# Optimization experiments

Hardware: AMD Instinct MI355X
Metric: run time of the kernel (lower is better)

## Reference

```python
import jax, jax.numpy as jnp
import numpy as np

TEMPERATURE = 8.0

def setup_inputs() -> dict:
    key = jax.random.key(0)
    kq, kk, kv, km = jax.random.split(key, 4)
    B, H, S, D = 4, 16, 2048, 64
    q = jax.random.normal(kq, (B, H, S, D), dtype=jnp.float32)
    k = jax.random.normal(kk, (B, H, S, D), dtype=jnp.float32)
    v = jax.random.normal(kv, (B, H, S, D), dtype=jnp.float32)
    mask = jax.random.randint(km, (B, S, S), 0, 2, dtype=jnp.int32)
    return {"q": q, "k": k, "v": v, "mask": mask}

def reference(q, k, v, mask):
    # attn = q @ k^T / temperature  -> [B, H, Sq, Sk]
    attn = jnp.einsum("bhqd,bhkd->bhqk", q, k) / TEMPERATURE
    mask0 = (mask == 0)[:, None, :, :]  # [B, 1, Sq, Sk]; True where masked out
    attn = jnp.where(mask0, -jnp.inf, attn)
    attn = jax.nn.softmax(attn, axis=-1)
    attn = jnp.where(mask0, 0.0, attn)
    output = jnp.einsum("bhqk,bhkd->bhqd", attn, v)
    return (output, attn)
```

## Files before the change

kernel.cpp:

```cpp
#include <hip/hip_runtime.h>
#include <cstdint>

#define B_ 4
#define H_ 16
#define S_ 2048
#define D_ 64

#define QSCALE (0.125f * 1.44269504088896f)

typedef _Float16 half8 __attribute__((ext_vector_type(8)));
typedef float f32x4 __attribute__((ext_vector_type(4)));
typedef float f32x16 __attribute__((ext_vector_type(16)));
typedef uint32_t u32x2 __attribute__((ext_vector_type(2)));
typedef uint32_t u32x4 __attribute__((ext_vector_type(4)));


__global__ void cvt_q_kernel(const float* __restrict__ q, _Float16* __restrict__ qh) {
    const int64_t N = (int64_t)B_ * H_ * S_ * D_;
    const int64_t step = (int64_t)gridDim.x * blockDim.x * 4;
    for (int64_t i = ((int64_t)blockIdx.x * blockDim.x + threadIdx.x) * 4; i < N; i += step) {
        float4 a = *reinterpret_cast<const float4*>(q + i);
        _Float16 ah[4] = { (_Float16)(a.x * QSCALE), (_Float16)(a.y * QSCALE),
                           (_Float16)(a.z * QSCALE), (_Float16)(a.w * QSCALE) };
        *reinterpret_cast<u32x2*>(qh + i) = *reinterpret_cast<u32x2*>(ah);
    }
}

__global__ void pack_k_kernel(const float* __restrict__ k, _Float16* __restrict__ kh) {
    const int bh = blockIdx.y;
    const int t = blockIdx.x;
    const int tid = threadIdx.x;
    const int kk = tid >> 6, lane = tid & 63, hi = lane >> 5, c = lane & 31;
    const float* src = k + ((int64_t)bh * S_ + t * 32 + c) * D_ + kk * 16 + hi * 8;
    float4 a = *reinterpret_cast<const float4*>(src);
    float4 b2 = *reinterpret_cast<const float4*>(src + 4);
    half8 h = { (_Float16)a.x, (_Float16)a.y, (_Float16)a.z, (_Float16)a.w,
                (_Float16)b2.x, (_Float16)b2.y, (_Float16)b2.z, (_Float16)b2.w };
    half8* dst = reinterpret_cast<half8*>(kh) + (((int64_t)bh * 64 + t) * 4 + kk) * 64 + hi * 32 + c;
    *dst = h;
}

__global__ void pack_v_kernel(const float* __restrict__ v, _Float16* __restrict__ vt) {
    const int bh = blockIdx.y;
    const int t = blockIdx.x;
    const int tid = threadIdx.x;
    const int g = tid >> 5, c = tid & 31;
    const int kk = g >> 2, hi = (g >> 1) & 1, db = g & 1;
    const float* src = v + ((int64_t)bh * S_ + t * 32 + kk * 16 + hi * 8) * D_ + c + 32 * db;
    half8 h;
#pragma unroll
    for (int j = 0; j < 8; ++j) h[j] = (_Float16)src[j * D_];
    half8* dst = reinterpret_cast<half8*>(vt) + (((int64_t)bh * 64 + t) * 8 + g) * 32 + c;
    *dst = h;
}

__global__ void pack_mask_kernel(const int* __restrict__ mask, uint32_t* __restrict__ mbits) {
    const int64_t groups = (int64_t)B_ * S_ * S_ / 64;
    const int lane = threadIdx.x & 63;
    const int64_t wstep = ((int64_t)gridDim.x * blockDim.x) >> 6;
    for (int64_t g = ((int64_t)blockIdx.x * blockDim.x + threadIdx.x) >> 6; g < groups; g += wstep) {
        int mv = mask[g * 64 + lane];
        unsigned long long bits = __ballot(mv != 0);
        if (lane == 0)
            *reinterpret_cast<unsigned long long*>(mbits + g * 2) = bits;
    }
}


__global__ __launch_bounds__(256, 2) void attn_fast(
    const _Float16* __restrict__ qh, const _Float16* __restrict__ kh, const _Float16* __restrict__ vt,
    const uint32_t* __restrict__ mbits,
    float* __restrict__ out, float* __restrict__ attn)
{
    const int tid = threadIdx.x;
    const int w = tid >> 6;
    const int lane = tid & 63;
    const int c = lane & 31;
    const int hi = lane >> 5;

    const int fid = blockIdx.x;
    const int xcd = fid & 7;
    const int slot = fid >> 3;
    const int p = xcd + 8 * (slot >> 4);
    const int x = slot & 15;
    const int b = p >> 4;

    const int qw = x * 128 + w * 32;
    const int64_t bh = p;
    const int64_t qrow = (int64_t)b * S_ + qw + c;

    half8 aq[4];
    {
        const _Float16* qp = qh + (bh * S_ + qw + c) * D_ + hi * 8;
#pragma unroll
        for (int kk = 0; kk < 4; ++kk)
            aq[kk] = *reinterpret_cast<const half8*>(qp + kk * 16);
    }

    const uint32_t* mrow = mbits + qrow * (S_ / 32);
    const half8* kbase = reinterpret_cast<const half8*>(kh) + (int64_t)bh * 64 * 4 * 64 + hi * 32 + c;
    const half8* vbase = reinterpret_cast<const half8*>(vt) + (int64_t)bh * 64 * 8 * 32 + c;

    auto LOADK = [&](half8 (&kr)[4], int t) {
        const half8* kp8 = kbase + (int64_t)t * 256;
#pragma unroll
        for (int kk = 0; kk < 4; ++kk) kr[kk] = kp8[kk * 64];
    };
    auto LOADV = [&](half8 (&vr)[4], int t) {
        const half8* vp8 = vbase + (int64_t)t * 256;
        vr[0] = vp8[(hi * 2 + 0) * 32];
        vr[1] = vp8[(hi * 2 + 1) * 32];
        vr[2] = vp8[(4 + hi * 2 + 0) * 32];
        vr[3] = vp8[(4 + hi * 2 + 1) * 32];
    };
    auto QK = [&](const half8 (&kr)[4]) -> f32x16 {
        f32x16 acc;
#pragma unroll
        for (int r = 0; r < 16; ++r) acc[r] = 0.f;
#pragma unroll
        for (int kk = 0; kk < 4; ++kk)
            acc = __builtin_amdgcn_mfma_f32_32x32x16_f16(kr[kk], aq[kk], acc, 0, 0, 0);
        return acc;
    };

    float l = 0.f;
    {
        auto bodyA = [&](const half8 (&kr)[4], uint32_t mwf) -> float {
            f32x16 acc = QK(kr);
            const uint32_t mw = mwf >> (hi * 4);
            float e[16];
#pragma unroll
            for (int r = 0; r < 16; ++r) {
                const bool dead = ((mw >> ((r & 3) + 8 * (r >> 2))) & 1u) == 0u;
                e[r] = __builtin_exp2f(dead ? -1e30f : acc[r]);
            }
#pragma unroll
            for (int st = 1; st < 16; st <<= 1)
#pragma unroll
                for (int i = 0; i < 16; i += 2 * st) e[i] += e[i + st];
            return e[0];
        };

        half8 ka[4], kb[4];
        uint32_t mA, mB;
        LOADK(ka, 0); mA = mrow[0];
        for (int t = 0; t < 64; t += 2) {
            LOADK(kb, t + 1); mB = mrow[t + 1];
            l += bodyA(ka, mA);
            if (t + 2 < 64) { LOADK(ka, t + 2); mA = mrow[t + 2]; }
            l += bodyA(kb, mB);
        }
    }
    const float lt = l + __shfl_xor(l, 32);
    const float rinv = 1.0f / lt;

    f32x16 o0, o1;
#pragma unroll
    for (int r = 0; r < 16; ++r) { o0[r] = 0.f; o1[r] = 0.f; }

    {
        auto bodyB = [&](const half8 (&kr)[4], const half8 (&vr)[4], uint32_t mwf, int t) {
            const int k0 = t * 32;
            f32x16 acc = QK(kr);
            const uint32_t mw = mwf >> (hi * 4);

            f32x4 pq0, pq1, pq2, pq3;
            uint32_t pk[8];
            {
#pragma unroll
                for (int e2 = 0; e2 < 4; ++e2) {
                    bool d0 = ((mw >> (0 + e2)) & 1u) == 0u;
                    bool d1 = ((mw >> (8 + e2)) & 1u) == 0u;
                    bool d2 = ((mw >> (16 + e2)) & 1u) == 0u;
                    bool d3 = ((mw >> (24 + e2)) & 1u) == 0u;
                    pq0[e2] = __builtin_exp2f(d0 ? -1e30f : acc[e2]) * rinv;
                    pq1[e2] = __builtin_exp2f(d1 ? -1e30f : acc[4 + e2]) * rinv;
                    pq2[e2] = __builtin_exp2f(d2 ? -1e30f : acc[8 + e2]) * rinv;
                    pq3[e2] = __builtin_exp2f(d3 ? -1e30f : acc[12 + e2]) * rinv;
                }
                pk[0] = __builtin_bit_cast(uint32_t, __builtin_amdgcn_cvt_pkrtz(pq0[0], pq0[1]));
                pk[1] = __builtin_bit_cast(uint32_t, __builtin_amdgcn_cvt_pkrtz(pq0[2], pq0[3]));
                pk[2] = __builtin_bit_cast(uint32_t, __builtin_amdgcn_cvt_pkrtz(pq1[0], pq1[1]));
                pk[3] = __builtin_bit_cast(uint32_t, __builtin_amdgcn_cvt_pkrtz(pq1[2], pq1[3]));
                pk[4] = __builtin_bit_cast(uint32_t, __builtin_amdgcn_cvt_pkrtz(pq2[0], pq2[1]));
                pk[5] = __builtin_bit_cast(uint32_t, __builtin_amdgcn_cvt_pkrtz(pq2[2], pq2[3]));
                pk[6] = __builtin_bit_cast(uint32_t, __builtin_amdgcn_cvt_pkrtz(pq3[0], pq3[1]));
                pk[7] = __builtin_bit_cast(uint32_t, __builtin_amdgcn_cvt_pkrtz(pq3[2], pq3[3]));
            }

            u32x2 rA = __builtin_amdgcn_permlane32_swap(pk[0], pk[2], false, false);
            u32x2 rB = __builtin_amdgcn_permlane32_swap(pk[1], pk[3], false, false);
            u32x2 rC = __builtin_amdgcn_permlane32_swap(pk[4], pk[6], false, false);
            u32x2 rD = __builtin_amdgcn_permlane32_swap(pk[5], pk[7], false, false);
            u32x4 fa0 = { rA[0], rB[0], rA[1], rB[1] };
            u32x4 fa1 = { rC[0], rD[0], rC[1], rD[1] };
            half8 pa0 = __builtin_bit_cast(half8, fa0);
            half8 pa1 = __builtin_bit_cast(half8, fa1);

            o0 = __builtin_amdgcn_mfma_f32_32x32x16_f16(pa0, vr[0], o0, 0, 0, 0);
            o1 = __builtin_amdgcn_mfma_f32_32x32x16_f16(pa0, vr[1], o1, 0, 0, 0);
            o0 = __builtin_amdgcn_mfma_f32_32x32x16_f16(pa1, vr[2], o0, 0, 0, 0);
            o1 = __builtin_amdgcn_mfma_f32_32x32x16_f16(pa1, vr[3], o1, 0, 0, 0);

            float* arow = attn + (bh * S_ + qw + c) * (int64_t)S_ + k0 + 4 * hi;
            *reinterpret_cast<f32x4*>(arow) = pq0;
            *reinterpret_cast<f32x4*>(arow + 8) = pq1;
            *reinterpret_cast<f32x4*>(arow + 16) = pq2;
            *reinterpret_cast<f32x4*>(arow + 24) = pq3;
        };

        half8 ka[4], kb[4], va[4], vb[4];
        uint32_t mA, mB;
        LOADK(ka, 0); LOADV(va, 0); mA = mrow[0];
        for (int t = 0; t < 64; t += 2) {
            LOADK(kb, t + 1); LOADV(vb, t + 1); mB = mrow[t + 1];
            bodyB(ka, va, mA, t);
            if (t + 2 < 64) { LOADK(ka, t + 2); LOADV(va, t + 2); mA = mrow[t + 2]; }
            bodyB(kb, vb, mB, t + 1);
        }
    }

#pragma unroll
    for (int r = 0; r < 16; ++r) {
        const int row = (r & 3) + 8 * (r >> 2) + 4 * hi;
        float* op = out + (bh * S_ + qw + row) * D_;
        op[c] = o0[r];
        op[c + 32] = o1[r];
    }
}

__global__ __launch_bounds__(256, 2) void attn_slow(
    const float* __restrict__ qf, const float* __restrict__ kf, const float* __restrict__ vf,
    const int* __restrict__ maskI, float* __restrict__ out, float* __restrict__ attn)
{
    const int tid = threadIdx.x;
    const int w = tid >> 6;
    const int lane = tid & 63;
    const int c = lane & 31;
    const int hi = lane >> 5;
    const int fid = blockIdx.x;
    const int p = fid & 63;
    const int x = fid >> 6;
    const int b = p >> 4;
    const int qw = x * 128 + w * 32;
    const int64_t bh = p;
    const int64_t qrow = (int64_t)b * S_ + qw + c;

    half8 aq[4];
    {
        const float* qp = qf + (bh * S_ + qw + c) * D_ + hi * 8;
#pragma unroll
        for (int kk = 0; kk < 4; ++kk)
#pragma unroll
            for (int j = 0; j < 8; ++j)
                aq[kk][j] = (_Float16)(qp[kk * 16 + j] * QSCALE);
    }

    float l = 0.f;
    for (int t = 0; t < 64; ++t) {
        const int k0 = t * 32;
        f32x16 acc;
#pragma unroll
        for (int r = 0; r < 16; ++r) acc[r] = 0.f;
        const float* kp = kf + (bh * S_ + k0 + c) * D_ + hi * 8;
#pragma unroll
        for (int kk = 0; kk < 4; ++kk) {
            half8 bk;
#pragma unroll
            for (int j = 0; j < 8; ++j) bk[j] = (_Float16)kp[kk * 16 + j];
            acc = __builtin_amdgcn_mfma_f32_32x32x16_f16(bk, aq[kk], acc, 0, 0, 0);
        }
        float e[16];
#pragma unroll
        for (int r = 0; r < 16; ++r) {
            const int key = k0 + (r & 3) + 8 * (r >> 2) + 4 * hi;
            const bool dead = maskI[qrow * S_ + key] == 0;
            e[r] = __builtin_exp2f(dead ? -1e30f : acc[r]);
        }
#pragma unroll
        for (int st = 1; st < 16; st <<= 1)
#pragma unroll
            for (int i = 0; i < 16; i += 2 * st) e[i] += e[i + st];
        l += e[0];
    }
    const float lt = l + __shfl_xor(l, 32);
    const float rinv = 1.0f / lt;

    f32x16 o0, o1;
#pragma unroll
    for (int r = 0; r < 16; ++r) { o0[r] = 0.f; o1[r] = 0.f; }

    for (int t = 0; t < 64; ++t) {
        const int k0 = t * 32;
        f32x16 acc;
#pragma unroll
        for (int r = 0; r < 16; ++r) acc[r] = 0.f;
        const float* kp = kf + (bh * S_ + k0 + c) * D_ + hi * 8;
#pragma unroll
        for (int kk = 0; kk < 4; ++kk) {
            half8 bk;
#pragma unroll
            for (int j = 0; j < 8; ++j) bk[j] = (_Float16)kp[kk * 16 + j];
            acc = __builtin_amdgcn_mfma_f32_32x32x16_f16(bk, aq[kk], acc, 0, 0, 0);
        }
        float* arow = attn + (bh * S_ + qw + c) * (int64_t)S_ + k0 + 4 * hi;
        uint32_t pk[8];
#pragma unroll
        for (int g4 = 0; g4 < 4; ++g4) {
            f32x4 pq;
#pragma unroll
            for (int e2 = 0; e2 < 4; ++e2) {
                const int key = k0 + e2 + 8 * g4 + 4 * hi;
                const bool dead = maskI[qrow * S_ + key] == 0;
                pq[e2] = __builtin_exp2f(dead ? -1e30f : acc[4 * g4 + e2]) * rinv;
            }
            *reinterpret_cast<f32x4*>(arow + 8 * g4) = pq;
            pk[2 * g4]     = __builtin_bit_cast(uint32_t, __builtin_amdgcn_cvt_pkrtz(pq[0], pq[1]));
            pk[2 * g4 + 1] = __builtin_bit_cast(uint32_t, __builtin_amdgcn_cvt_pkrtz(pq[2], pq[3]));
        }
        u32x2 rA = __builtin_amdgcn_permlane32_swap(pk[0], pk[2], false, false);
        u32x2 rB = __builtin_amdgcn_permlane32_swap(pk[1], pk[3], false, false);
        u32x2 rC = __builtin_amdgcn_permlane32_swap(pk[4], pk[6], false, false);
        u32x2 rD = __builtin_amdgcn_permlane32_swap(pk[5], pk[7], false, false);
        u32x4 fa0 = { rA[0], rB[0], rA[1], rB[1] };
        u32x4 fa1 = { rC[0], rD[0], rC[1], rD[1] };
        half8 pa0 = __builtin_bit_cast(half8, fa0);
        half8 pa1 = __builtin_bit_cast(half8, fa1);

        half8 bv00, bv01, bv10, bv11;
        const float* vp0 = vf + (bh * S_ + k0 + hi * 8) * D_ + c;
        const float* vp1 = vp0 + 16 * D_;
#pragma unroll
        for (int j = 0; j < 8; ++j) {
            bv00[j] = (_Float16)vp0[j * D_];
            bv01[j] = (_Float16)vp0[j * D_ + 32];
            bv10[j] = (_Float16)vp1[j * D_];
            bv11[j] = (_Float16)vp1[j * D_ + 32];
        }
        o0 = __builtin_amdgcn_mfma_f32_32x32x16_f16(pa0, bv00, o0, 0, 0, 0);
        o1 = __builtin_amdgcn_mfma_f32_32x32x16_f16(pa0, bv01, o1, 0, 0, 0);
        o0 = __builtin_amdgcn_mfma_f32_32x32x16_f16(pa1, bv10, o0, 0, 0, 0);
        o1 = __builtin_amdgcn_mfma_f32_32x32x16_f16(pa1, bv11, o1, 0, 0, 0);
    }

#pragma unroll
    for (int r = 0; r < 16; ++r) {
        const int row = (r & 3) + 8 * (r >> 2) + 4 * hi;
        float* op = out + (bh * S_ + qw + row) * D_;
        op[c] = o0[r];
        op[c + 32] = o1[r];
    }
}

extern "C" void kernel_launch(void* const* d_in, const int* in_sizes, int n_in,
                              void* d_out, int out_size, void* d_ws, size_t ws_size,
                              hipStream_t stream) {
    const float* q = (const float*)d_in[0];
    const float* k = (const float*)d_in[1];
    const float* v = (const float*)d_in[2];
    const int* mask = (const int*)d_in[3];
    float* out = (float*)d_out;
    float* attn = out + (int64_t)B_ * H_ * S_ * D_;

    const size_t nElem = (size_t)B_ * H_ * S_ * D_;
    const size_t maskWords = (size_t)B_ * S_ * (S_ / 32);
    const size_t need = nElem * 2 * 3 + maskWords * 4;

    const int nblk = B_ * H_ * (S_ / 128);
    if (d_ws != nullptr && ws_size >= need) {
        _Float16* qh = (_Float16*)d_ws;
        _Float16* kh = qh + nElem;
        _Float16* vt = kh + nElem;
        uint32_t* mb = (uint32_t*)(vt + nElem);
        cvt_q_kernel<<<1024, 256, 0, stream>>>(q, qh);
        pack_k_kernel<<<dim3(S_ / 32, B_ * H_), 256, 0, stream>>>(k, kh);
        pack_v_kernel<<<dim3(S_ / 32, B_ * H_), 256, 0, stream>>>(v, vt);
        pack_mask_kernel<<<2048, 256, 0, stream>>>(mask, mb);
        attn_fast<<<nblk, 256, 0, stream>>>(qh, kh, vt, mb, out, attn);
    } else {
        attn_slow<<<nblk, 256, 0, stream>>>(q, k, v, mask, out, attn);
    }
}
```

Baseline: 546.1 us.

## Transpose packed mask bits for coalesced loads and deepen K/V prefetch pipeline

The packed mask is stored transposed so that, for each key tile, the 32 query-row words sit next to each other and a wavefront's mask loads coalesce instead of striding by the full row length. The first pass now keeps four K tiles and the second pass three K/V tiles in flight, issuing each next load right after the MFMAs rather than one tile ahead. The aim is to hide global-load latency behind compute in this bandwidth-heavy kernel. The cost is higher register pressure under launch_bounds(256,2), which could cause spills, plus a more scattered write pattern in the mask pack kernel.

Measured after the change: 545.4 us. Within noise of the previous version (-0.1%).

```diff
diff --git a/kernel.cpp b/kernel.cpp
--- a/kernel.cpp
+++ b/kernel.cpp
@@ -54,22 +54,29 @@
     *dst = h;
 }
 
-__global__ void pack_mask_kernel(const int* __restrict__ mask, uint32_t* __restrict__ mbits) {
+__global__ void pack_mask_kernel(const int* __restrict__ mask, uint32_t* __restrict__ mbT) {
     const int64_t groups = (int64_t)B_ * S_ * S_ / 64;
     const int lane = threadIdx.x & 63;
     const int64_t wstep = ((int64_t)gridDim.x * blockDim.x) >> 6;
     for (int64_t g = ((int64_t)blockIdx.x * blockDim.x + threadIdx.x) >> 6; g < groups; g += wstep) {
         int mv = mask[g * 64 + lane];
         unsigned long long bits = __ballot(mv != 0);
-        if (lane == 0)
-            *reinterpret_cast<unsigned long long*>(mbits + g * 2) = bits;
+        if (lane == 0) {
+            const int u = (int)(g & 31);
+            const int64_t bq = g >> 5;
+            const int q = (int)(bq & (S_ - 1));
+            const int b = (int)(bq >> 11);
+            const int64_t base = (((int64_t)b * 64 + (q >> 5)) * 64) * 32 + (q & 31);
+            mbT[base + (int64_t)(2 * u) * 32]     = (uint32_t)bits;
+            mbT[base + (int64_t)(2 * u + 1) * 32] = (uint32_t)(bits >> 32);
+        }
     }
 }
 
 
 __global__ __launch_bounds__(256, 2) void attn_fast(
     const _Float16* __restrict__ qh, const _Float16* __restrict__ kh, const _Float16* __restrict__ vt,
-    const uint32_t* __restrict__ mbits,
+    const uint32_t* __restrict__ mbT,
     float* __restrict__ out, float* __restrict__ attn)
 {
     const int tid = threadIdx.x;
@@ -87,7 +94,6 @@
 
     const int qw = x * 128 + w * 32;
     const int64_t bh = p;
-    const int64_t qrow = (int64_t)b * S_ + qw + c;
 
     half8 aq[4];
     {
@@ -97,7 +103,7 @@
             aq[kk] = *reinterpret_cast<const half8*>(qp + kk * 16);
     }
 
-    const uint32_t* mrow = mbits + qrow * (S_ / 32);
+    const uint32_t* mT = mbT + (((int64_t)b * 64 + x * 4 + w) * 64) * 32 + c;
     const half8* kbase = reinterpret_cast<const half8*>(kh) + (int64_t)bh * 64 * 4 * 64 + hi * 32 + c;
     const half8* vbase = reinterpret_cast<const half8*>(vt) + (int64_t)bh * 64 * 8 * 32 + c;
 
@@ -141,14 +147,17 @@
             return e[0];
         };
 
-        half8 ka[4], kb[4];
-        uint32_t mA, mB;
-        LOADK(ka, 0); mA = mrow[0];
-        for (int t = 0; t < 64; t += 2) {
-            LOADK(kb, t + 1); mB = mrow[t + 1];
-            l += bodyA(ka, mA);
-            if (t + 2 < 64) { LOADK(ka, t + 2); mA = mrow[t + 2]; }
-            l += bodyA(kb, mB);
+        half8 k0_[4], k1_[4], k2_[4], k3_[4];
+        uint32_t m0, m1, m2, m3;
+        LOADK(k0_, 0); m0 = mT[0 * 32];
+        LOADK(k1_, 1); m1 = mT[1 * 32];
+        LOADK(k2_, 2); m2 = mT[2 * 32];
+        LOADK(k3_, 3); m3 = mT[3 * 32];
+        for (int t = 0; t < 64; t += 4) {
+            l += bodyA(k0_, m0); if (t + 4 < 64) { LOADK(k0_, t + 4); m0 = mT[(t + 4) * 32]; }
+            l += bodyA(k1_, m1); if (t + 5 < 64) { LOADK(k1_, t + 5); m1 = mT[(t + 5) * 32]; }
+            l += bodyA(k2_, m2); if (t + 6 < 64) { LOADK(k2_, t + 6); m2 = mT[(t + 6) * 32]; }
+            l += bodyA(k3_, m3); if (t + 7 < 64) { LOADK(k3_, t + 7); m3 = mT[(t + 7) * 32]; }
         }
     }
     const float lt = l + __shfl_xor(l, 32);
@@ -159,34 +168,32 @@
     for (int r = 0; r < 16; ++r) { o0[r] = 0.f; o1[r] = 0.f; }
 
     {
-        auto bodyB = [&](const half8 (&kr)[4], const half8 (&vr)[4], uint32_t mwf, int t) {
+        auto stepB = [&](half8 (&K)[4], half8 (&V)[4], uint32_t& m_, int t, int tn) {
             const int k0 = t * 32;
-            f32x16 acc = QK(kr);
-            const uint32_t mw = mwf >> (hi * 4);
+            f32x16 acc = QK(K);
+            const uint32_t mw = m_ >> (hi * 4);
 
             f32x4 pq0, pq1, pq2, pq3;
             uint32_t pk[8];
-            {
-#pragma unroll
-                for (int e2 = 0; e2 < 4; ++e2) {
-                    bool d0 = ((mw >> (0 + e2)) & 1u) == 0u;
-                    bool d1 = ((mw >> (8 + e2)) & 1u) == 0u;
-                    bool d2 = ((mw >> (16 + e2)) & 1u) == 0u;
-                    bool d3 = ((mw >> (24 + e2)) & 1u) == 0u;
-                    pq0[e2] = __builtin_exp2f(d0 ? -1e30f : acc[e2]) * rinv;
-                    pq1[e2] = __builtin_exp2f(d1 ? -1e30f : acc[4 + e2]) * rinv;
-                    pq2[e2] = __builtin_exp2f(d2 ? -1e30f : acc[8 + e2]) * rinv;
-                    pq3[e2] = __builtin_exp2f(d3 ? -1e30f : acc[12 + e2]) * rinv;
-                }
-                pk[0] = __builtin_bit_cast(uint32_t, __builtin_amdgcn_cvt_pkrtz(pq0[0], pq0[1]));
-                pk[1] = __builtin_bit_cast(uint32_t, __builtin_amdgcn_cvt_pkrtz(pq0[2], pq0[3]));
-                pk[2] = __builtin_bit_cast(uint32_t, __builtin_amdgcn_cvt_pkrtz(pq1[0], pq1[1]));
-                pk[3] = __builtin_bit_cast(uint32_t, __builtin_amdgcn_cvt_pkrtz(pq1[2], pq1[3]));
-                pk[4] = __builtin_bit_cast(uint32_t, __builtin_amdgcn_cvt_pkrtz(pq2[0], pq2[1]));
-                pk[5] = __builtin_bit_cast(uint32_t, __builtin_amdgcn_cvt_pkrtz(pq2[2], pq2[3]));
-                pk[6] = __builtin_bit_cast(uint32_t, __builtin_amdgcn_cvt_pkrtz(pq3[0], pq3[1]));
-                pk[7] = __builtin_bit_cast(uint32_t, __builtin_amdgcn_cvt_pkrtz(pq3[2], pq3[3]));
+#pragma unroll
+            for (int e2 = 0; e2 < 4; ++e2) {
+                bool d0 = ((mw >> (0 + e2)) & 1u) == 0u;
+                bool d1 = ((mw >> (8 + e2)) & 1u) == 0u;
+                bool d2 = ((mw >> (16 + e2)) & 1u) == 0u;
+                bool d3 = ((mw >> (24 + e2)) & 1u) == 0u;
+                pq0[e2] = __builtin_exp2f(d0 ? -1e30f : acc[e2]) * rinv;
+                pq1[e2] = __builtin_exp2f(d1 ? -1e30f : acc[4 + e2]) * rinv;
+                pq2[e2] = __builtin_exp2f(d2 ? -1e30f : acc[8 + e2]) * rinv;
+                pq3[e2] = __builtin_exp2f(d3 ? -1e30f : acc[12 + e2]) * rinv;
             }
+            pk[0] = __builtin_bit_cast(uint32_t, __builtin_amdgcn_cvt_pkrtz(pq0[0], pq0[1]));
+            pk[1] = __builtin_bit_cast(uint32_t, __builtin_amdgcn_cvt_pkrtz(pq0[2], pq0[3]));
+            pk[2] = __builtin_bit_cast(uint32_t, __builtin_amdgcn_cvt_pkrtz(pq1[0], pq1[1]));
+            pk[3] = __builtin_bit_cast(uint32_t, __builtin_amdgcn_cvt_pkrtz(pq1[2], pq1[3]));
+            pk[4] = __builtin_bit_cast(uint32_t, __builtin_amdgcn_cvt_pkrtz(pq2[0], pq2[1]));
+            pk[5] = __builtin_bit_cast(uint32_t, __builtin_amdgcn_cvt_pkrtz(pq2[2], pq2[3]));
+            pk[6] = __builtin_bit_cast(uint32_t, __builtin_amdgcn_cvt_pkrtz(pq3[0], pq3[1]));
+            pk[7] = __builtin_bit_cast(uint32_t, __builtin_amdgcn_cvt_pkrtz(pq3[2], pq3[3]));
 
             u32x2 rA = __builtin_amdgcn_permlane32_swap(pk[0], pk[2], false, false);
             u32x2 rB = __builtin_amdgcn_permlane32_swap(pk[1], pk[3], false, false);
@@ -197,10 +204,12 @@
             half8 pa0 = __builtin_bit_cast(half8, fa0);
             half8 pa1 = __builtin_bit_cast(half8, fa1);
 
-            o0 = __builtin_amdgcn_mfma_f32_32x32x16_f16(pa0, vr[0], o0, 0, 0, 0);
-            o1 = __builtin_amdgcn_mfma_f32_32x32x16_f16(pa0, vr[1], o1, 0, 0, 0);
-            o0 = __builtin_amdgcn_mfma_f32_32x32x16_f16(pa1, vr[2], o0, 0, 0, 0);
-            o1 = __builtin_amdgcn_mfma_f32_32x32x16_f16(pa1, vr[3], o1, 0, 0, 0);
+            o0 = __builtin_amdgcn_mfma_f32_32x32x16_f16(pa0, V[0], o0, 0, 0, 0);
+            o1 = __builtin_amdgcn_mfma_f32_32x32x16_f16(pa0, V[1], o1, 0, 0, 0);
+            o0 = __builtin_amdgcn_mfma_f32_32x32x16_f16(pa1, V[2], o0, 0, 0, 0);
+            o1 = __builtin_amdgcn_mfma_f32_32x32x16_f16(pa1, V[3], o1, 0, 0, 0);
+
+            if (tn < 64) { LOADK(K, tn); LOADV(V, tn); m_ = mT[tn * 32]; }
 
             float* arow = attn + (bh * S_ + qw + c) * (int64_t)S_ + k0 + 4 * hi;
             *reinterpret_cast<f32x4*>(arow) = pq0;
@@ -209,15 +218,17 @@
             *reinterpret_cast<f32x4*>(arow + 24) = pq3;
         };
 
-        half8 ka[4], kb[4], va[4], vb[4];
-        uint32_t mA, mB;
-        LOADK(ka, 0); LOADV(va, 0); mA = mrow[0];
-        for (int t = 0; t < 64; t += 2) {
-            LOADK(kb, t + 1); LOADV(vb, t + 1); mB = mrow[t + 1];
-            bodyB(ka, va, mA, t);
-            if (t + 2 < 64) { LOADK(ka, t + 2); LOADV(va, t + 2); mA = mrow[t + 2]; }
-            bodyB(kb, vb, mB, t + 1);
-        }
+        half8 Ka[4], Kb[4], Kc[4], Va[4], Vb[4], Vc[4];
+        uint32_t ma, mb_, mc;
+        LOADK(Ka, 0); LOADV(Va, 0); ma = mT[0 * 32];
+        LOADK(Kb, 1); LOADV(Vb, 1); mb_ = mT[1 * 32];
+        LOADK(Kc, 2); LOADV(Vc, 2); mc = mT[2 * 32];
+        for (int t = 0; t < 63; t += 3) {
+            stepB(Ka, Va, ma, t, t + 3);
+            stepB(Kb, Vb, mb_, t + 1, t + 4);
+            stepB(Kc, Vc, mc, t + 2, t + 5);
+        }
+        stepB(Ka, Va, ma, 63, 64);
     }
 
 #pragma unroll
@@ -371,12 +382,12 @@
         _Float16* qh = (_Float16*)d_ws;
         _Float16* kh = qh + nElem;
         _Float16* vt = kh + nElem;
-        uint32_t* mb = (uint32_t*)(vt + nElem);
+        uint32_t* mbT = (uint32_t*)(vt + nElem);
         cvt_q_kernel<<<1024, 256, 0, stream>>>(q, qh);
         pack_k_kernel<<<dim3(S_ / 32, B_ * H_), 256, 0, stream>>>(k, kh);
         pack_v_kernel<<<dim3(S_ / 32, B_ * H_), 256, 0, stream>>>(v, vt);
-        pack_mask_kernel<<<2048, 256, 0, stream>>>(mask, mb);
-        attn_fast<<<nblk, 256, 0, stream>>>(qh, kh, vt, mb, out, attn);
+        pack_mask_kernel<<<2048, 256, 0, stream>>>(mask, mbT);
+        attn_fast<<<nblk, 256, 0, stream>>>(qh, kh, vt, mbT, out, attn);
     } else {
         attn_slow<<<nblk, 256, 0, stream>>>(q, k, v, mask, out, attn);
     }
```
